# Performance work log

Hardware: AMD Instinct MI355X
Metric: run time of the kernel (lower is better)

The kernel has to match this reference:

```python
import jax, jax.numpy as jnp
import numpy as np

EPS = 1e-6
BASE_LR = 0.01


def setup_inputs() -> dict:
    key = jax.random.key(0)
    ks = jax.random.split(key, 4)
    B, H, T, K, D = 4, 16, 512, 16, 64
    return {
        "XQ": jax.random.normal(ks[0], (B, H, T, K, D), dtype=jnp.float32),
        "XK": jax.random.normal(ks[1], (B, H, T, K, D), dtype=jnp.float32),
        "XV": jax.random.normal(ks[2], (B, H, T, K, D), dtype=jnp.float32),
        "W1": 0.02 * jax.random.normal(ks[3], (H, D, D), dtype=jnp.float32),
        "b1": jnp.zeros((H, 1, D), dtype=jnp.float32),
        "gamma": jnp.ones((H, D), dtype=jnp.float32),
        "beta": jnp.zeros((H, D), dtype=jnp.float32),
    }


def reference(XQ, XK, XV, W1, b1, gamma, beta):
    # XQ/XK/XV: [B, H, T, K, D]  (T mini-batches of size K per sequence)
    B, H, T, K, D = XQ.shape
    g = gamma.reshape(1, H, 1, D)
    be = beta.reshape(1, H, 1, D)

    def ln(x):  # LayerNorm over last dim, biased variance, eps=1e-6
        mu = x.mean(-1, keepdims=True)
        var = ((x - mu) ** 2).mean(-1, keepdims=True)
        return g * ((x - mu) * jax.lax.rsqrt(var + EPS)) + be

    # get_eta: eta = base_lr / (1 + ||x||), clamp norm at 1e-6 -> [B,H,T,K,1]
    nrm = jnp.maximum(jnp.linalg.norm(XK, axis=-1, keepdims=True), EPS)
    eta = BASE_LR / (1.0 + nrm)

    W1_0 = jnp.broadcast_to(W1[None], (B, H, D, D))
    b1_0 = jnp.broadcast_to(b1[None], (B, H, 1, D))

    # scan over the T mini-batches (sequential TTT inner-loop updates)
    xs = tuple(jnp.moveaxis(a, 2, 0) for a in (XQ, XK, XV, eta))

    def step(carry, x):
        W1c, b1c = carry          # [B,H,D,D], [B,H,1,D]
        xq, xk, xv, et = x        # [B,H,K,D], ..., [B,H,K,1]
        Z1 = jnp.einsum('bhkd,bhdf->bhkf', xk, W1c) + b1c
        grad_Z1 = 2.0 * (ln(Z1) - (xv - xk))
        grad_W1 = jnp.einsum('bhkd,bhkf->bhdf', xk, grad_Z1)
        grad_b1 = grad_Z1.sum(axis=2, keepdims=True)
        # mean_k(eta_k * grad) == mean(eta) * grad since grad is k-independent
        em = et.mean(axis=2, keepdims=True)  # [B,H,1,1]
        W1u = W1c - em * grad_W1
        b1u = b1c - em * grad_b1
        Z1d = jnp.einsum('bhkd,bhdf->bhkf', xq, W1u) + b1u
        out = xq + ln(Z1d)
        # carry update uses only the last token of the mini-batch
        el = et[:, :, -1:, :]  # [B,H,1,1]
        gWl = jnp.einsum('bhkd,bhkf->bhdf', xk[:, :, -1:, :], grad_Z1[:, :, -1:, :])
        W1n = W1c - el * gWl
        b1n = b1c - el * grad_Z1[:, :, -1:, :]
        return (W1n, b1n), out

    _, outs = jax.lax.scan(step, (W1_0, b1_0), xs)
    return jnp.moveaxis(outs, 0, 2)  # [B,H,T,K,D]
```

## Files before the change

### kernel.cpp

```cpp
#include <hip/hip_runtime.h>

#define T_STEPS 512
#define NTHREADS 1024
#define EPSF 1e-6f
#define BASE_LR_F 0.01f

__device__ __forceinline__ float lane_bcast(float v, int l) {
    return __int_as_float(__builtin_amdgcn_readlane(__float_as_int(v), l));
}

__device__ __forceinline__ float wave_sum1(float a) {
    #pragma unroll
    for (int m = 16; m >= 1; m >>= 1) a += __shfl_xor(a, m, 64);
    return lane_bcast(a, 0) + lane_bcast(a, 32);
}
__device__ __forceinline__ void wave_sum2(float &a, float &b) {
    #pragma unroll
    for (int m = 16; m >= 1; m >>= 1) {
        a += __shfl_xor(a, m, 64);
        b += __shfl_xor(b, m, 64);
    }
    a = lane_bcast(a, 0) + lane_bcast(a, 32);
    b = lane_bcast(b, 0) + lane_bcast(b, 32);
}

struct SMem {
    float W[64][64];
    float b1s[64];
    __align__(16) float xk[16][68];
    __align__(16) float xq[16][68];
    __align__(16) float gz[16][68];
    __align__(16) float eta[16];
};

__global__ __launch_bounds__(NTHREADS, 4) void ttt_kernel(
    const float* __restrict__ XQ, const float* __restrict__ XK,
    const float* __restrict__ XV, const float* __restrict__ W1,
    const float* __restrict__ b1, const float* __restrict__ gamma,
    const float* __restrict__ beta, float* __restrict__ OUT)
{
    __shared__ SMem sm;

    const int bh  = blockIdx.x;
    const int h   = bh & 15;
    const int tid = threadIdx.x;
    const int f   = tid & 63;
    const int q   = tid >> 6;

    {
        float* zp = (float*)&sm;
        const int nflt = (int)(sizeof(SMem) / 4);
        for (int i = tid; i < nflt; i += NTHREADS) zp[i] = 0.0f;
    }
    __syncthreads();

    for (int i = tid; i < 4096; i += NTHREADS)
        sm.W[i >> 6][i & 63] = W1[h * 4096 + i];
    if (tid < 64) sm.b1s[tid] = b1[h * 64 + tid];
    const float g_f  = gamma[h * 64 + f];
    const float be_f = beta[h * 64 + f];

    const int base   = bh * (T_STEPS * 1024);
    const int rowoff = q * 64 + f;

    float xkr = XK[base + rowoff];
    float xqr = XQ[base + rowoff];
    float xvr = XV[base + rowoff];
    float nxk = 0.0f, nxq = 0.0f, nxv = 0.0f;

    __syncthreads();

    for (int t = 0; t < T_STEPS; ++t) {
        if (t + 1 < T_STEPS) {
            const int o1 = base + (t + 1) * 1024 + rowoff;
            nxk = XK[o1]; nxq = XQ[o1]; nxv = XV[o1];
        }

        sm.xk[q][f] = xkr;
        sm.xq[q][f] = xqr;
        {
            const float s = wave_sum1(xkr * xkr);
            if (f == 0) {
                const float nrm = fmaxf(sqrtf(s), EPSF);
                sm.eta[q] = BASE_LR_F / (1.0f + nrm);
            }
        }
        __syncthreads();

        float em, el;
        {
            const float4 e0 = *(const float4*)&sm.eta[0];
            const float4 e1 = *(const float4*)&sm.eta[4];
            const float4 e2 = *(const float4*)&sm.eta[8];
            const float4 e3 = *(const float4*)&sm.eta[12];
            em = ((e0.x+e0.y+e0.z+e0.w) + (e1.x+e1.y+e1.z+e1.w)
                + (e2.x+e2.y+e2.z+e2.w) + (e3.x+e3.y+e3.z+e3.w)) * (1.0f/16.0f);
            el = e3.w;
        }
        const float bb = sm.b1s[f];
        const float4 xk15b = *(const float4*)&sm.xk[15][4 * q];

        float acc  = bb;
        float accd = 0.0f;
        #pragma unroll
        for (int i = 0; i < 16; ++i) {
            const float4 k4 = *(const float4*)&sm.xk[q][4 * i];
            const float4 q4 = *(const float4*)&sm.xq[q][4 * i];
            const float w0 = sm.W[4*i+0][f];
            const float w1 = sm.W[4*i+1][f];
            const float w2 = sm.W[4*i+2][f];
            const float w3 = sm.W[4*i+3][f];
            acc  = fmaf(k4.x, w0, acc );  accd = fmaf(q4.x, w0, accd);
            acc  = fmaf(k4.y, w1, acc );  accd = fmaf(q4.y, w1, accd);
            acc  = fmaf(k4.z, w2, acc );  accd = fmaf(q4.z, w2, accd);
            acc  = fmaf(k4.w, w3, acc );  accd = fmaf(q4.w, w3, accd);
        }

        float coef;
        {
            const int kk = f & 15, tt = f >> 4;
            float a = 0.0f;
            #pragma unroll
            for (int c = 0; c < 4; ++c) {
                const float4 xq4 = *(const float4*)&sm.xq[q][16 * tt + 4 * c];
                const float4 xk4 = *(const float4*)&sm.xk[kk][16 * tt + 4 * c];
                a = fmaf(xq4.x, xk4.x, a); a = fmaf(xq4.y, xk4.y, a);
                a = fmaf(xq4.z, xk4.z, a); a = fmaf(xq4.w, xk4.w, a);
            }
            a += __shfl_xor(a, 16, 64);
            a += __shfl_xor(a, 32, 64);
            coef = em * (1.0f + a);
        }

        {
            float s1 = acc, s2 = acc * acc;
            wave_sum2(s1, s2);
            const float mu  = s1 * (1.0f/64.0f);
            const float var = s2 * (1.0f/64.0f) - mu * mu;
            const float inv = rsqrtf(var + EPSF);
            const float lnv = g_f * ((acc - mu) * inv) + be_f;
            sm.gz[q][f] = 2.0f * (lnv - (xvr - xkr));
        }
        __syncthreads();

        float zd = accd + bb;
        #pragma unroll
        for (int kk = 0; kk < 16; ++kk)
            zd = fmaf(-lane_bcast(coef, kk), sm.gz[kk][f], zd);

        {
            float s1 = zd, s2 = zd * zd;
            wave_sum2(s1, s2);
            const float mu  = s1 * (1.0f/64.0f);
            const float var = s2 * (1.0f/64.0f) - mu * mu;
            const float inv = rsqrtf(var + EPSF);
            const float lnv = g_f * ((zd - mu) * inv) + be_f;
            OUT[base + t * 1024 + rowoff] = xqr + lnv;
        }

        {
            const float c2 = el * sm.gz[15][f];
            sm.W[4*q+0][f] = fmaf(-xk15b.x, c2, sm.W[4*q+0][f]);
            sm.W[4*q+1][f] = fmaf(-xk15b.y, c2, sm.W[4*q+1][f]);
            sm.W[4*q+2][f] = fmaf(-xk15b.z, c2, sm.W[4*q+2][f]);
            sm.W[4*q+3][f] = fmaf(-xk15b.w, c2, sm.W[4*q+3][f]);
            if (q == 0) sm.b1s[f] = bb - c2;
        }

        xkr = nxk; xqr = nxq; xvr = nxv;
    }
}

extern "C" void kernel_launch(void* const* d_in, const int* in_sizes, int n_in,
                              void* d_out, int out_size, void* d_ws, size_t ws_size,
                              hipStream_t stream) {
    const float* XQ    = (const float*)d_in[0];
    const float* XK    = (const float*)d_in[1];
    const float* XV    = (const float*)d_in[2];
    const float* W1    = (const float*)d_in[3];
    const float* b1    = (const float*)d_in[4];
    const float* gamma = (const float*)d_in[5];
    const float* beta  = (const float*)d_in[6];
    float* OUT = (float*)d_out;
    ttt_kernel<<<dim3(64), dim3(NTHREADS), 0, stream>>>(
        XQ, XK, XV, W1, b1, gamma, beta, OUT);
}
```

Measured before the change: 2.648 ms.

## Keep the W1 column in per-thread registers instead of shared memory

Each thread now holds its full 64-entry column of the fast weight W in registers, so the per-step matvecs no longer read 64 W values from LDS. Every wave redundantly applies the rank-1 carry update to its own copy, using a double-buffered shared copy of the last xk row, and the bias is likewise kept in a register. The two dot products are split across two accumulators to shorten the FMA dependency chains. In exchange each thread does 64 update FMAs per step instead of 4 and needs far more registers, which risks spilling under the 1024-thread launch bound.

Result: faster. 2.461 ms (-7.1%).

```diff
diff --git a/kernel.cpp b/kernel.cpp
--- a/kernel.cpp
+++ b/kernel.cpp
@@ -25,11 +25,10 @@
 }
 
 struct SMem {
-    float W[64][64];
-    float b1s[64];
     __align__(16) float xk[16][68];
     __align__(16) float xq[16][68];
     __align__(16) float gz[16][68];
+    __align__(16) float xk15c[2][64];
     __align__(16) float eta[16];
 };
 
@@ -52,11 +51,11 @@
         const int nflt = (int)(sizeof(SMem) / 4);
         for (int i = tid; i < nflt; i += NTHREADS) zp[i] = 0.0f;
     }
-    __syncthreads();
 
-    for (int i = tid; i < 4096; i += NTHREADS)
-        sm.W[i >> 6][i & 63] = W1[h * 4096 + i];
-    if (tid < 64) sm.b1s[tid] = b1[h * 64 + tid];
+    float Wreg[64];
+    #pragma unroll
+    for (int d = 0; d < 64; ++d) Wreg[d] = W1[h * 4096 + d * 64 + f];
+    float b1r = b1[h * 64 + f];
     const float g_f  = gamma[h * 64 + f];
     const float be_f = beta[h * 64 + f];
 
@@ -78,6 +77,7 @@
 
         sm.xk[q][f] = xkr;
         sm.xq[q][f] = xqr;
+        if (q == 15) sm.xk15c[t & 1][f] = xkr;
         {
             const float s = wave_sum1(xkr * xkr);
             if (f == 0) {
@@ -97,24 +97,26 @@
                 + (e2.x+e2.y+e2.z+e2.w) + (e3.x+e3.y+e3.z+e3.w)) * (1.0f/16.0f);
             el = e3.w;
         }
-        const float bb = sm.b1s[f];
-        const float4 xk15b = *(const float4*)&sm.xk[15][4 * q];
 
-        float acc  = bb;
-        float accd = 0.0f;
+        float ac0 = 0.0f, ac1 = 0.0f, ad0 = 0.0f, ad1 = 0.0f;
         #pragma unroll
         for (int i = 0; i < 16; ++i) {
             const float4 k4 = *(const float4*)&sm.xk[q][4 * i];
             const float4 q4 = *(const float4*)&sm.xq[q][4 * i];
-            const float w0 = sm.W[4*i+0][f];
-            const float w1 = sm.W[4*i+1][f];
-            const float w2 = sm.W[4*i+2][f];
-            const float w3 = sm.W[4*i+3][f];
-            acc  = fmaf(k4.x, w0, acc );  accd = fmaf(q4.x, w0, accd);
-            acc  = fmaf(k4.y, w1, acc );  accd = fmaf(q4.y, w1, accd);
-            acc  = fmaf(k4.z, w2, acc );  accd = fmaf(q4.z, w2, accd);
-            acc  = fmaf(k4.w, w3, acc );  accd = fmaf(q4.w, w3, accd);
+            if (i & 1) {
+                ac1 = fmaf(k4.x, Wreg[4*i+0], ac1); ad1 = fmaf(q4.x, Wreg[4*i+0], ad1);
+                ac1 = fmaf(k4.y, Wreg[4*i+1], ac1); ad1 = fmaf(q4.y, Wreg[4*i+1], ad1);
+                ac1 = fmaf(k4.z, Wreg[4*i+2], ac1); ad1 = fmaf(q4.z, Wreg[4*i+2], ad1);
+                ac1 = fmaf(k4.w, Wreg[4*i+3], ac1); ad1 = fmaf(q4.w, Wreg[4*i+3], ad1);
+            } else {
+                ac0 = fmaf(k4.x, Wreg[4*i+0], ac0); ad0 = fmaf(q4.x, Wreg[4*i+0], ad0);
+                ac0 = fmaf(k4.y, Wreg[4*i+1], ac0); ad0 = fmaf(q4.y, Wreg[4*i+1], ad0);
+                ac0 = fmaf(k4.z, Wreg[4*i+2], ac0); ad0 = fmaf(q4.z, Wreg[4*i+2], ad0);
+                ac0 = fmaf(k4.w, Wreg[4*i+3], ac0); ad0 = fmaf(q4.w, Wreg[4*i+3], ad0);
+            }
         }
+        const float acc  = b1r + (ac0 + ac1);
+        const float accd = ad0 + ad1;
 
         float coef;
         {
@@ -143,7 +145,7 @@
         }
         __syncthreads();
 
-        float zd = accd + bb;
+        float zd = accd + b1r;
         #pragma unroll
         for (int kk = 0; kk < 16; ++kk)
             zd = fmaf(-lane_bcast(coef, kk), sm.gz[kk][f], zd);
@@ -160,11 +162,15 @@
 
         {
             const float c2 = el * sm.gz[15][f];
-            sm.W[4*q+0][f] = fmaf(-xk15b.x, c2, sm.W[4*q+0][f]);
-            sm.W[4*q+1][f] = fmaf(-xk15b.y, c2, sm.W[4*q+1][f]);
-            sm.W[4*q+2][f] = fmaf(-xk15b.z, c2, sm.W[4*q+2][f]);
-            sm.W[4*q+3][f] = fmaf(-xk15b.w, c2, sm.W[4*q+3][f]);
-            if (q == 0) sm.b1s[f] = bb - c2;
+            #pragma unroll
+            for (int i = 0; i < 16; ++i) {
+                const float4 x4 = *(const float4*)&sm.xk15c[t & 1][4 * i];
+                Wreg[4*i+0] = fmaf(-x4.x, c2, Wreg[4*i+0]);
+                Wreg[4*i+1] = fmaf(-x4.y, c2, Wreg[4*i+1]);
+                Wreg[4*i+2] = fmaf(-x4.z, c2, Wreg[4*i+2]);
+                Wreg[4*i+3] = fmaf(-x4.w, c2, Wreg[4*i+3]);
+            }
+            b1r -= c2;
         }
 
         xkr = nxk; xqr = nxq; xvr = nxv;
```
